# Kernel optimization log

Measured on AMD Instinct MI355X. Metric: run time of the kernel, lower is better.

Reference implementation:

```python
import jax, jax.numpy as jnp
import numpy as np

N_TF = 11
H = 1024
B = 2048


def setup_inputs() -> dict:
    key = jax.random.key(0)
    ks = jax.random.split(key, 10)
    s = 0.02  # weight init scale
    return {
        "h_stack": jax.random.normal(ks[0], (B, N_TF, H), dtype=jnp.float32),
        "base_confidence": jax.random.uniform(ks[1], (B,), dtype=jnp.float32),
        "kW1": jax.random.normal(ks[2], (H, H // 2), dtype=jnp.float32) * s,
        "kb1": jnp.zeros((H // 2,), jnp.float32),
        "kW2": jax.random.normal(ks[3], (H // 2, 1), dtype=jnp.float32) * s,
        "kb2": jnp.zeros((1,), jnp.float32),
        "lW1": jax.random.normal(ks[4], (H, H // 2), dtype=jnp.float32) * s,
        "lb1": jnp.zeros((H // 2,), jnp.float32),
        "lW2": jax.random.normal(ks[5], (H // 2, 1), dtype=jnp.float32) * s,
        "lb2": jnp.zeros((1,), jnp.float32),
        "dW1": jax.random.normal(ks[6], (2 * H, H), dtype=jnp.float32) * s,
        "db1": jnp.zeros((H,), jnp.float32),
        "dW2": jax.random.normal(ks[7], (H, 1), dtype=jnp.float32) * s,
        "db2": jnp.zeros((1,), jnp.float32),
        "kinetic_weight": jnp.asarray(1.0, jnp.float32),
        "local_weight": jnp.asarray(0.5, jnp.float32),
        "interaction_weight": jnp.asarray(0.3, jnp.float32),
        "temperature": jnp.asarray(1.0, jnp.float32),
    }


def reference(h_stack, base_confidence, kW1, kb1, kW2, kb2, lW1, lb1, lW2, lb2,
              dW1, db1, dW2, db2, kinetic_weight, local_weight,
              interaction_weight, temperature):
    n_tf = h_stack.shape[1]
    h = h_stack.shape[2]
    ii, jj = np.triu_indices(n_tf, k=1)  # 55 upper-triangular pairs
    dist_w = jnp.asarray(1.0 / (np.abs(ii - jj) + 1.0), dtype=h_stack.dtype)
    n_pairs = ii.shape[0]

    # kinetic: mean over TFs of small MLP, negated
    k_hid = jax.nn.relu(jnp.einsum('bth,hd->btd', h_stack, kW1) + kb1)
    k_per = (jnp.einsum('btd,do->bto', k_hid, kW2) + kb2)[..., 0]  # [B, T]
    kinetic_energy = -kinetic_weight * k_per.mean(axis=1)

    # local: relu of per-TF MLP, mean
    l_hid = jax.nn.relu(jnp.einsum('bth,hd->btd', h_stack, lW1) + lb1)
    l_per = (jnp.einsum('btd,do->bto', l_hid, lW2) + lb2)[..., 0]
    local_energy = local_weight * jax.nn.relu(l_per).mean(axis=1)

    # interaction: concat-MLP over all pairs, batched.
    # cat([h_i, h_j]) @ dW1 == h_i @ dW1[:H] + h_j @ dW1[H:]
    dW1a, dW1b = dW1[:h], dW1[h:]
    pre_i = jnp.einsum('bth,hd->btd', h_stack, dW1a)  # [B, T, H]
    pre_j = jnp.einsum('bth,hd->btd', h_stack, dW1b)  # [B, T, H]
    hid = jax.nn.relu(pre_i[:, ii] + pre_j[:, jj] + db1)  # [B, P, H]
    dis = jax.nn.relu((jnp.einsum('bpd,do->bpo', hid, dW2) + db2)[..., 0])  # [B, P]
    interaction_energy = interaction_weight * (dis * dist_w).sum(axis=1) / n_pairs

    total_energy = kinetic_energy + local_energy + interaction_energy
    energy_confidence = jax.nn.sigmoid(-total_energy / (jnp.abs(temperature) + 0.1))
    adjusted_confidence = base_confidence * energy_confidence
    return jnp.stack([total_energy, kinetic_energy, local_energy,
                      interaction_energy, energy_confidence,
                      adjusted_confidence], axis=0)  # [6, B]
```

## Files before the change

kernel.cpp:

```cpp
#include <hip/hip_runtime.h>
#include <hip/hip_bf16.h>
#include <math.h>

typedef __attribute__((ext_vector_type(8))) short bf16x8;
typedef __attribute__((ext_vector_type(4))) float f32x4;

#define NBATCH   2048
#define GB       4
#define ROWS     44
#define ROWSP    48
#define LDSA_BYTES (ROWSP * 1024 * 2)
#define STG_TILE   (ROWSP * 20)
#define STG_WAVE   (2 * STG_TILE)
#define LDS_TOTAL  (LDSA_BYTES + 8 * STG_WAVE * 4)

__device__ unsigned short g_wsB2[(size_t)3072 * 1024];

__device__ float g_ws2[(size_t)NBATCH * 128];

static constexpr int II_[55] = {
    0,0,0,0,0,0,0,0,0,0, 1,1,1,1,1,1,1,1,1, 2,2,2,2,2,2,2,2,
    3,3,3,3,3,3,3, 4,4,4,4,4,4, 5,5,5,5,5, 6,6,6,6, 7,7,7, 8,8, 9};
static constexpr int JJ_[55] = {
    1,2,3,4,5,6,7,8,9,10, 2,3,4,5,6,7,8,9,10, 3,4,5,6,7,8,9,10,
    4,5,6,7,8,9,10, 5,6,7,8,9,10, 6,7,8,9,10, 7,8,9,10, 8,9,10, 9,10, 10};

__device__ __forceinline__ unsigned short f32_to_bf16u(float f) {
    unsigned u = __float_as_uint(f);
    u += 0x7fffu + ((u >> 16) & 1u);
    return (unsigned short)(u >> 16);
}

__global__ void pack_weights(const float* __restrict__ kW1,
                             const float* __restrict__ lW1,
                             const float* __restrict__ dW1) {
    const int t = blockIdx.x * 256 + threadIdx.x;
    const int lane = t & 63;
    const int kk   = (t >> 6) & 31;
    const int g    = t >> 11;
    const int col  = g * 16 + (lane & 15);
    const int k0   = kk * 32 + (lane >> 4) * 8;
    const float* src; int ncol, c;
    if (col < 512)       { src = kW1;                          ncol = 512;  c = col; }
    else if (col < 1024) { src = lW1;                          ncol = 512;  c = col - 512; }
    else if (col < 2048) { src = dW1;                          ncol = 1024; c = col - 1024; }
    else                 { src = dW1 + (size_t)1024 * 1024;    ncol = 1024; c = col - 2048; }
    bf16x8 v;
    #pragma unroll
    for (int j = 0; j < 8; ++j)
        v[j] = (short)f32_to_bf16u(src[(size_t)(k0 + j) * ncol + c]);
    *(bf16x8*)(g_wsB2 + (size_t)t * 8) = v;
}

__launch_bounds__(512, 2)
__global__ void energy_mfma(
    const float* __restrict__ h_stack,
    const float* __restrict__ kb1, const float* __restrict__ kW2,
    const float* __restrict__ lb1, const float* __restrict__ lW2,
    const float* __restrict__ db1, const float* __restrict__ dW2)
{
    extern __shared__ char smem[];
    char* Ab = smem;
    float* stageBase = (float*)(smem + LDSA_BYTES);

    const int tid  = threadIdx.x;
    const int wv   = tid >> 6;
    const int ln   = tid & 63;
    const int lo16 = ln & 15;
    const int hi4  = ln >> 4;
    const unsigned xorv = (unsigned)((ln & 7) << 4);

    const int bx = blockIdx.x;
    const int x  = bx & 7;
    const int colHalf  = x & 1;
    const int rowBlock = (bx >> 3) * 4 + (x >> 1);

    {
        const size_t hbase = (size_t)rowBlock * (ROWS * 1024);
        #pragma unroll
        for (int i = 0; i < 11; ++i) {
            int idx = tid + i * 512;
            int row = idx >> 7;
            int kc  = idx & 127;
            const float* src = h_stack + hbase + (size_t)row * 1024 + kc * 8;
            float4 a = *(const float4*)src;
            float4 b = *(const float4*)(src + 4);
            bf16x8 v;
            v[0] = (short)f32_to_bf16u(a.x); v[1] = (short)f32_to_bf16u(a.y);
            v[2] = (short)f32_to_bf16u(a.z); v[3] = (short)f32_to_bf16u(a.w);
            v[4] = (short)f32_to_bf16u(b.x); v[5] = (short)f32_to_bf16u(b.y);
            v[6] = (short)f32_to_bf16u(b.z); v[7] = (short)f32_to_bf16u(b.w);
            unsigned kbyte = ((unsigned)(kc * 16)) ^ ((unsigned)((row & 7) << 4));
            *(bf16x8*)(Ab + row * 2048 + kbyte) = v;
        }
        {
            int row = ROWS + (tid >> 7);
            int kc  = tid & 127;
            unsigned kbyte = ((unsigned)(kc * 16)) ^ ((unsigned)((row & 7) << 4));
            bf16x8 z = {0,0,0,0,0,0,0,0};
            *(bf16x8*)(Ab + row * 2048 + kbyte) = z;
        }
    }
    __syncthreads();

    float kin_part = 0.f, loc_part = 0.f;
    float accP[55];
    #pragma unroll
    for (int p = 0; p < 55; ++p) accP[p] = 0.f;

    float* stg0 = stageBase + wv * STG_WAVE;
    float* stg1 = stg0 + STG_TILE;

    auto readA = [&](int m, int kk) -> bf16x8 {
        unsigned addr = (unsigned)((16 * m + lo16) * 2048)
                      + ((unsigned)(kk * 64 + hi4 * 16) ^ xorv);
        return *(const bf16x8*)(Ab + addr);
    };

    #pragma unroll 1
    for (int ui = 0; ui < 3; ++ui) {
        const int u = 24 * colHalf + ui * 8 + wv;
        int g0, g1, g2, g3;
        if (u < 16) { g0 = 4 * u; g1 = 4 * u + 1; g2 = 4 * u + 2; g3 = 4 * u + 3; }
        else        { int v = u - 16;
                      g0 = 64 + 2 * v; g1 = 128 + 2 * v;
                      g2 = 65 + 2 * v; g3 = 129 + 2 * v; }

        const unsigned short* bp0 = g_wsB2 + (size_t)g0 * 16384 + ln * 8;
        const unsigned short* bp1 = g_wsB2 + (size_t)g1 * 16384 + ln * 8;
        const unsigned short* bp2 = g_wsB2 + (size_t)g2 * 16384 + ln * 8;
        const unsigned short* bp3 = g_wsB2 + (size_t)g3 * 16384 + ln * 8;

        f32x4 acc[4][3];
        #pragma unroll
        for (int q = 0; q < 4; ++q)
            #pragma unroll
            for (int m = 0; m < 3; ++m) acc[q][m] = (f32x4){0.f, 0.f, 0.f, 0.f};

        auto ldB = [&](const unsigned short* p, int kk) -> bf16x8 {
            return *(const bf16x8*)(p + (size_t)kk * 512);
        };
        auto mfma12 = [&](bf16x8 a0, bf16x8 a1, bf16x8 a2,
                          bf16x8 b0, bf16x8 b1, bf16x8 b2, bf16x8 b3) {
            acc[0][0] = __builtin_amdgcn_mfma_f32_16x16x32_bf16(a0, b0, acc[0][0], 0, 0, 0);
            acc[0][1] = __builtin_amdgcn_mfma_f32_16x16x32_bf16(a1, b0, acc[0][1], 0, 0, 0);
            acc[0][2] = __builtin_amdgcn_mfma_f32_16x16x32_bf16(a2, b0, acc[0][2], 0, 0, 0);
            acc[1][0] = __builtin_amdgcn_mfma_f32_16x16x32_bf16(a0, b1, acc[1][0], 0, 0, 0);
            acc[1][1] = __builtin_amdgcn_mfma_f32_16x16x32_bf16(a1, b1, acc[1][1], 0, 0, 0);
            acc[1][2] = __builtin_amdgcn_mfma_f32_16x16x32_bf16(a2, b1, acc[1][2], 0, 0, 0);
            acc[2][0] = __builtin_amdgcn_mfma_f32_16x16x32_bf16(a0, b2, acc[2][0], 0, 0, 0);
            acc[2][1] = __builtin_amdgcn_mfma_f32_16x16x32_bf16(a1, b2, acc[2][1], 0, 0, 0);
            acc[2][2] = __builtin_amdgcn_mfma_f32_16x16x32_bf16(a2, b2, acc[2][2], 0, 0, 0);
            acc[3][0] = __builtin_amdgcn_mfma_f32_16x16x32_bf16(a0, b3, acc[3][0], 0, 0, 0);
            acc[3][1] = __builtin_amdgcn_mfma_f32_16x16x32_bf16(a1, b3, acc[3][1], 0, 0, 0);
            acc[3][2] = __builtin_amdgcn_mfma_f32_16x16x32_bf16(a2, b3, acc[3][2], 0, 0, 0);
        };

        bf16x8 A0 = readA(0, 0), A1 = readA(1, 0), A2 = readA(2, 0);
        bf16x8 B0 = ldB(bp0, 0), B1 = ldB(bp1, 0), B2 = ldB(bp2, 0), B3 = ldB(bp3, 0);
        bf16x8 C0 = ldB(bp0, 1), C1 = ldB(bp1, 1), C2 = ldB(bp2, 1), C3 = ldB(bp3, 1);

        #pragma unroll 2
        for (int kk = 0; kk < 31; ++kk) {
            bf16x8 a0 = A0, a1 = A1, a2 = A2;
            A0 = readA(0, kk + 1); A1 = readA(1, kk + 1); A2 = readA(2, kk + 1);
            bf16x8 b0 = B0, b1 = B1, b2 = B2, b3 = B3;
            B0 = C0; B1 = C1; B2 = C2; B3 = C3;
            if (kk < 30) {
                C0 = ldB(bp0, kk + 2); C1 = ldB(bp1, kk + 2);
                C2 = ldB(bp2, kk + 2); C3 = ldB(bp3, kk + 2);
            }
            mfma12(a0, a1, a2, b0, b1, b2, b3);
        }
        mfma12(A0, A1, A2, B0, B1, B2, B3);

        if (u < 16) {
            const float* b1arr = (u < 8) ? kb1 : lb1;
            const float* w2arr = (u < 8) ? kW2 : lW2;
            const int colrel0 = (u < 8) ? u * 64 : (u - 8) * 64;
            float part = 0.f;
            #pragma unroll
            for (int q = 0; q < 4; ++q) {
                const int colrel = colrel0 + q * 16 + lo16;
                const float b1v = b1arr[colrel];
                const float w2v = w2arr[colrel];
                float* sb = (q & 1) ? stg1 : stg0;
                #pragma unroll
                for (int m = 0; m < 3; ++m)
                    #pragma unroll
                    for (int r = 0; r < 4; ++r) {
                        const int row = 16 * m + 4 * hi4 + r;
                        sb[row * 20 + lo16] = fmaxf(acc[q][m][r] + b1v, 0.f) * w2v;
                    }
                asm volatile("s_waitcnt lgkmcnt(0)" ::: "memory");
                if (ln < ROWS) {
                    const f32x4* rp = (const f32x4*)(sb + ln * 20);
                    float s = 0.f;
                    #pragma unroll
                    for (int c4 = 0; c4 < 4; ++c4) {
                        f32x4 vv = rp[c4];
                        s += vv[0] + vv[1] + vv[2] + vv[3];
                    }
                    part += s;
                }
            }
            if (u < 8) kin_part += part; else loc_part += part;
        } else {
            const int v = u - 16;
            #pragma unroll
            for (int half = 0; half < 2; ++half) {
                const int dcol = (2 * v + half) * 16 + lo16;
                const float db1v = db1[dcol];
                const float dw2v = dW2[dcol];
                #pragma unroll
                for (int m = 0; m < 3; ++m)
                    #pragma unroll
                    for (int r = 0; r < 4; ++r) {
                        const int row = 16 * m + 4 * hi4 + r;
                        stg0[row * 20 + lo16] = acc[2 * half + 0][m][r];
                        stg1[row * 20 + lo16] = acc[2 * half + 1][m][r];
                    }
                asm volatile("s_waitcnt lgkmcnt(0)" ::: "memory");
                float pi[11], pj[11];
                #pragma unroll
                for (int t = 0; t < 11; ++t) {
                    const int row = 11 * hi4 + t;
                    pi[t] = stg0[row * 20 + lo16] + db1v;
                    pj[t] = stg1[row * 20 + lo16];
                }
                asm volatile("s_waitcnt lgkmcnt(0)" ::: "memory");
                #pragma unroll
                for (int p = 0; p < 55; ++p) {
                    const float s = pi[II_[p]] + pj[JJ_[p]];
                    accP[p] = fmaf(fmaxf(s, 0.f), dw2v, accP[p]);
                }
            }
        }
    }

    __syncthreads();
    float* kinbuf  = stageBase;
    float* locbuf  = stageBase + 512;
    float* pairbuf = stageBase + 1024;
    float* kinrow  = stageBase + 3040;
    float* locrow  = stageBase + 3104;

    kinbuf[wv * 64 + ln] = kin_part;
    locbuf[wv * 64 + ln] = loc_part;
    #pragma unroll
    for (int p = 0; p < 55; ++p) {
        float vsum = accP[p];
        vsum += __shfl_xor(vsum, 1);
        vsum += __shfl_xor(vsum, 2);
        vsum += __shfl_xor(vsum, 4);
        vsum += __shfl_xor(vsum, 8);
        if (lo16 == 0) pairbuf[wv * 224 + hi4 * 56 + p] = vsum;
    }
    __syncthreads();

    if (tid < 220) {
        const int b = tid / 55, p = tid % 55;
        float s = 0.f;
        #pragma unroll
        for (int w = 0; w < 8; ++w) s += pairbuf[w * 224 + b * 56 + p];
        const int gb = rowBlock * 4 + b;
        g_ws2[(size_t)gb * 128 + (colHalf ? 67 : 12) + p] = s;
    }
    if (colHalf == 0) {
        if (tid >= 256 && tid < 304) {
            const int r = tid - 256;
            float sk = 0.f, sl = 0.f;
            #pragma unroll
            for (int w = 0; w < 8; ++w) { sk += kinbuf[w * 64 + r]; sl += locbuf[w * 64 + r]; }
            kinrow[r] = sk; locrow[r] = sl;
        }
        __syncthreads();
        if (tid < 4) {
            const int b = tid;
            const int gb = rowBlock * 4 + b;
            float ks = 0.f;
            #pragma unroll
            for (int t = 0; t < 11; ++t) ks += kinrow[11 * b + t];
            g_ws2[(size_t)gb * 128 + 0] = ks;
            #pragma unroll
            for (int t = 0; t < 11; ++t)
                g_ws2[(size_t)gb * 128 + 1 + t] = locrow[11 * b + t];
        }
    }
}

__global__ void finalize(
    const float* __restrict__ base_conf,
    const float* __restrict__ kb2, const float* __restrict__ lb2,
    const float* __restrict__ db2,
    const float* __restrict__ kwp, const float* __restrict__ lwp,
    const float* __restrict__ iwp, const float* __restrict__ tmpp,
    float* __restrict__ out)
{
    const int gb = blockIdx.x * 256 + threadIdx.x;
    if (gb >= NBATCH) return;
    const float* w = g_ws2 + (size_t)gb * 128;
    const float kw = kwp[0], lw = lwp[0], iw = iwp[0], temp = tmpp[0];

    const float kinetic = -kw * (w[0] * (1.f / 11.f) + kb2[0]);

    float ls = 0.f;
    #pragma unroll
    for (int t = 0; t < 11; ++t) ls += fmaxf(w[1 + t] + lb2[0], 0.f);
    const float local_e = lw * (ls * (1.f / 11.f));

    float is = 0.f;
    #pragma unroll
    for (int p = 0; p < 55; ++p) {
        float s = w[12 + p] + w[67 + p] + db2[0];
        s = fmaxf(s, 0.f);
        is += s * (1.f / (float)(JJ_[p] - II_[p] + 1));
    }
    const float inter = iw * (is * (1.f / 55.f));

    const float total = kinetic + local_e + inter;
    const float ec = 1.f / (1.f + expf(total / (fabsf(temp) + 0.1f)));
    out[0 * NBATCH + gb] = total;
    out[1 * NBATCH + gb] = kinetic;
    out[2 * NBATCH + gb] = local_e;
    out[3 * NBATCH + gb] = inter;
    out[4 * NBATCH + gb] = ec;
    out[5 * NBATCH + gb] = base_conf[gb] * ec;
}

extern "C" void kernel_launch(void* const* d_in, const int* in_sizes, int n_in,
                              void* d_out, int out_size, void* d_ws, size_t ws_size,
                              hipStream_t stream) {
    const float* h_stack   = (const float*)d_in[0];
    const float* base_conf = (const float*)d_in[1];
    const float* kW1 = (const float*)d_in[2];
    const float* kb1 = (const float*)d_in[3];
    const float* kW2 = (const float*)d_in[4];
    const float* kb2 = (const float*)d_in[5];
    const float* lW1 = (const float*)d_in[6];
    const float* lb1 = (const float*)d_in[7];
    const float* lW2 = (const float*)d_in[8];
    const float* lb2 = (const float*)d_in[9];
    const float* dW1 = (const float*)d_in[10];
    const float* db1 = (const float*)d_in[11];
    const float* dW2 = (const float*)d_in[12];
    const float* db2 = (const float*)d_in[13];
    const float* kwp = (const float*)d_in[14];
    const float* lwp = (const float*)d_in[15];
    const float* iwp = (const float*)d_in[16];
    const float* tmpp= (const float*)d_in[17];
    float* out = (float*)d_out;

    hipLaunchKernelGGL(pack_weights, dim3(1536), dim3(256), 0, stream, kW1, lW1, dW1);

    hipFuncSetAttribute((const void*)energy_mfma,
                        hipFuncAttributeMaxDynamicSharedMemorySize, LDS_TOTAL);
    hipLaunchKernelGGL(energy_mfma, dim3(1024), dim3(512), LDS_TOTAL, stream,
                       h_stack, kb1, kW2, lb1, lW2, db1, dW2);

    hipLaunchKernelGGL(finalize, dim3(8), dim3(256), 0, stream,
                       base_conf, kb2, lb2, db2, kwp, lwp, iwp, tmpp, out);
}
```

Baseline: 289.2 us.

## Make energy kernel loop over four row blocks per workgroup

The grid shrinks from 1024 to 256 workgroups, and each workgroup now processes four consecutive row blocks in sequence. Each block gets its own h_stack staging, MFMA pass and reduction, with barriers between blocks. Launch bounds are relaxed to one workgroup per CU so the compiler has more registers, and h_stack is read with nontemporal loads. The aim is to cut workgroup launch and tail overhead and reduce register pressure, but staging the next block is still serialized with compute.

```diff
diff --git a/kernel.cpp b/kernel.cpp
--- a/kernel.cpp
+++ b/kernel.cpp
@@ -6,7 +6,6 @@
 typedef __attribute__((ext_vector_type(4))) float f32x4;
 
 #define NBATCH   2048
-#define GB       4
 #define ROWS     44
 #define ROWSP    48
 #define LDSA_BYTES (ROWSP * 1024 * 2)
@@ -29,6 +28,10 @@
     unsigned u = __float_as_uint(f);
     u += 0x7fffu + ((u >> 16) & 1u);
     return (unsigned short)(u >> 16);
+}
+
+__device__ __forceinline__ f32x4 ldnt(const float* p) {
+    return __builtin_nontemporal_load((const f32x4*)p);
 }
 
 __global__ void pack_weights(const float* __restrict__ kW1,
@@ -52,7 +55,7 @@
     *(bf16x8*)(g_wsB2 + (size_t)t * 8) = v;
 }
 
-__launch_bounds__(512, 2)
+__launch_bounds__(512, 1)
 __global__ void energy_mfma(
     const float* __restrict__ h_stack,
     const float* __restrict__ kb1, const float* __restrict__ kW2,
@@ -72,41 +75,39 @@
 
     const int bx = blockIdx.x;
     const int x  = bx & 7;
-    const int colHalf  = x & 1;
-    const int rowBlock = (bx >> 3) * 4 + (x >> 1);
-
-    {
-        const size_t hbase = (size_t)rowBlock * (ROWS * 1024);
+    const int colHalf = x & 1;
+    const int hidx    = (bx >> 3) * 4 + (x >> 1);
+    const int rbBase  = hidx * 4;
+
+    auto stageA = [&](int rb) {
+        const size_t hbase = (size_t)rb * (ROWS * 1024);
         #pragma unroll
         for (int i = 0; i < 11; ++i) {
             int idx = tid + i * 512;
             int row = idx >> 7;
             int kc  = idx & 127;
             const float* src = h_stack + hbase + (size_t)row * 1024 + kc * 8;
-            float4 a = *(const float4*)src;
-            float4 b = *(const float4*)(src + 4);
+            f32x4 a = ldnt(src);
+            f32x4 b = ldnt(src + 4);
             bf16x8 v;
-            v[0] = (short)f32_to_bf16u(a.x); v[1] = (short)f32_to_bf16u(a.y);
-            v[2] = (short)f32_to_bf16u(a.z); v[3] = (short)f32_to_bf16u(a.w);
-            v[4] = (short)f32_to_bf16u(b.x); v[5] = (short)f32_to_bf16u(b.y);
-            v[6] = (short)f32_to_bf16u(b.z); v[7] = (short)f32_to_bf16u(b.w);
+            v[0] = (short)f32_to_bf16u(a[0]); v[1] = (short)f32_to_bf16u(a[1]);
+            v[2] = (short)f32_to_bf16u(a[2]); v[3] = (short)f32_to_bf16u(a[3]);
+            v[4] = (short)f32_to_bf16u(b[0]); v[5] = (short)f32_to_bf16u(b[1]);
+            v[6] = (short)f32_to_bf16u(b[2]); v[7] = (short)f32_to_bf16u(b[3]);
             unsigned kbyte = ((unsigned)(kc * 16)) ^ ((unsigned)((row & 7) << 4));
             *(bf16x8*)(Ab + row * 2048 + kbyte) = v;
         }
-        {
-            int row = ROWS + (tid >> 7);
-            int kc  = tid & 127;
-            unsigned kbyte = ((unsigned)(kc * 16)) ^ ((unsigned)((row & 7) << 4));
-            bf16x8 z = {0,0,0,0,0,0,0,0};
-            *(bf16x8*)(Ab + row * 2048 + kbyte) = z;
-        }
+    };
+
+    {
+        int row = ROWS + (tid >> 7);
+        int kc  = tid & 127;
+        unsigned kbyte = ((unsigned)(kc * 16)) ^ ((unsigned)((row & 7) << 4));
+        bf16x8 z = {0,0,0,0,0,0,0,0};
+        *(bf16x8*)(Ab + row * 2048 + kbyte) = z;
     }
+    stageA(rbBase);
     __syncthreads();
-
-    float kin_part = 0.f, loc_part = 0.f;
-    float accP[55];
-    #pragma unroll
-    for (int p = 0; p < 55; ++p) accP[p] = 0.f;
 
     float* stg0 = stageBase + wv * STG_WAVE;
     float* stg1 = stg0 + STG_TILE;
@@ -118,173 +119,189 @@
     };
 
     #pragma unroll 1
-    for (int ui = 0; ui < 3; ++ui) {
-        const int u = 24 * colHalf + ui * 8 + wv;
-        int g0, g1, g2, g3;
-        if (u < 16) { g0 = 4 * u; g1 = 4 * u + 1; g2 = 4 * u + 2; g3 = 4 * u + 3; }
-        else        { int v = u - 16;
-                      g0 = 64 + 2 * v; g1 = 128 + 2 * v;
-                      g2 = 65 + 2 * v; g3 = 129 + 2 * v; }
-
-        const unsigned short* bp0 = g_wsB2 + (size_t)g0 * 16384 + ln * 8;
-        const unsigned short* bp1 = g_wsB2 + (size_t)g1 * 16384 + ln * 8;
-        const unsigned short* bp2 = g_wsB2 + (size_t)g2 * 16384 + ln * 8;
-        const unsigned short* bp3 = g_wsB2 + (size_t)g3 * 16384 + ln * 8;
-
-        f32x4 acc[4][3];
+    for (int item = 0; item < 4; ++item) {
+        const int rb = rbBase + item;
+
+        float kin_part = 0.f, loc_part = 0.f;
+        float accP[55];
         #pragma unroll
-        for (int q = 0; q < 4; ++q)
+        for (int p = 0; p < 55; ++p) accP[p] = 0.f;
+
+        #pragma unroll 1
+        for (int ui = 0; ui < 3; ++ui) {
+            const int u = 24 * colHalf + ui * 8 + wv;
+            int g0, g1, g2, g3;
+            if (u < 16) { g0 = 4 * u; g1 = 4 * u + 1; g2 = 4 * u + 2; g3 = 4 * u + 3; }
+            else        { int v = u - 16;
+                          g0 = 64 + 2 * v; g1 = 128 + 2 * v;
+                          g2 = 65 + 2 * v; g3 = 129 + 2 * v; }
+
+            const unsigned short* bp0 = g_wsB2 + (size_t)g0 * 16384 + ln * 8;
+            const unsigned short* bp1 = g_wsB2 + (size_t)g1 * 16384 + ln * 8;
+            const unsigned short* bp2 = g_wsB2 + (size_t)g2 * 16384 + ln * 8;
+            const unsigned short* bp3 = g_wsB2 + (size_t)g3 * 16384 + ln * 8;
+
+            f32x4 acc[4][3];
             #pragma unroll
-            for (int m = 0; m < 3; ++m) acc[q][m] = (f32x4){0.f, 0.f, 0.f, 0.f};
-
-        auto ldB = [&](const unsigned short* p, int kk) -> bf16x8 {
-            return *(const bf16x8*)(p + (size_t)kk * 512);
-        };
-        auto mfma12 = [&](bf16x8 a0, bf16x8 a1, bf16x8 a2,
-                          bf16x8 b0, bf16x8 b1, bf16x8 b2, bf16x8 b3) {
-            acc[0][0] = __builtin_amdgcn_mfma_f32_16x16x32_bf16(a0, b0, acc[0][0], 0, 0, 0);
-            acc[0][1] = __builtin_amdgcn_mfma_f32_16x16x32_bf16(a1, b0, acc[0][1], 0, 0, 0);
-            acc[0][2] = __builtin_amdgcn_mfma_f32_16x16x32_bf16(a2, b0, acc[0][2], 0, 0, 0);
-            acc[1][0] = __builtin_amdgcn_mfma_f32_16x16x32_bf16(a0, b1, acc[1][0], 0, 0, 0);
-            acc[1][1] = __builtin_amdgcn_mfma_f32_16x16x32_bf16(a1, b1, acc[1][1], 0, 0, 0);
-            acc[1][2] = __builtin_amdgcn_mfma_f32_16x16x32_bf16(a2, b1, acc[1][2], 0, 0, 0);
-            acc[2][0] = __builtin_amdgcn_mfma_f32_16x16x32_bf16(a0, b2, acc[2][0], 0, 0, 0);
-            acc[2][1] = __builtin_amdgcn_mfma_f32_16x16x32_bf16(a1, b2, acc[2][1], 0, 0, 0);
-            acc[2][2] = __builtin_amdgcn_mfma_f32_16x16x32_bf16(a2, b2, acc[2][2], 0, 0, 0);
-            acc[3][0] = __builtin_amdgcn_mfma_f32_16x16x32_bf16(a0, b3, acc[3][0], 0, 0, 0);
-            acc[3][1] = __builtin_amdgcn_mfma_f32_16x16x32_bf16(a1, b3, acc[3][1], 0, 0, 0);
-            acc[3][2] = __builtin_amdgcn_mfma_f32_16x16x32_bf16(a2, b3, acc[3][2], 0, 0, 0);
-        };
-
-        bf16x8 A0 = readA(0, 0), A1 = readA(1, 0), A2 = readA(2, 0);
-        bf16x8 B0 = ldB(bp0, 0), B1 = ldB(bp1, 0), B2 = ldB(bp2, 0), B3 = ldB(bp3, 0);
-        bf16x8 C0 = ldB(bp0, 1), C1 = ldB(bp1, 1), C2 = ldB(bp2, 1), C3 = ldB(bp3, 1);
-
-        #pragma unroll 2
-        for (int kk = 0; kk < 31; ++kk) {
-            bf16x8 a0 = A0, a1 = A1, a2 = A2;
-            A0 = readA(0, kk + 1); A1 = readA(1, kk + 1); A2 = readA(2, kk + 1);
-            bf16x8 b0 = B0, b1 = B1, b2 = B2, b3 = B3;
-            B0 = C0; B1 = C1; B2 = C2; B3 = C3;
-            if (kk < 30) {
-                C0 = ldB(bp0, kk + 2); C1 = ldB(bp1, kk + 2);
-                C2 = ldB(bp2, kk + 2); C3 = ldB(bp3, kk + 2);
+            for (int q = 0; q < 4; ++q)
+                #pragma unroll
+                for (int m = 0; m < 3; ++m) acc[q][m] = (f32x4){0.f, 0.f, 0.f, 0.f};
+
+            auto ldB = [&](const unsigned short* p, int kk) -> bf16x8 {
+                return *(const bf16x8*)(p + (size_t)kk * 512);
+            };
+            auto mfma12 = [&](bf16x8 a0, bf16x8 a1, bf16x8 a2,
+                              bf16x8 b0, bf16x8 b1, bf16x8 b2, bf16x8 b3) {
+                acc[0][0] = __builtin_amdgcn_mfma_f32_16x16x32_bf16(a0, b0, acc[0][0], 0, 0, 0);
+                acc[0][1] = __builtin_amdgcn_mfma_f32_16x16x32_bf16(a1, b0, acc[0][1], 0, 0, 0);
+                acc[0][2] = __builtin_amdgcn_mfma_f32_16x16x32_bf16(a2, b0, acc[0][2], 0, 0, 0);
+                acc[1][0] = __builtin_amdgcn_mfma_f32_16x16x32_bf16(a0, b1, acc[1][0], 0, 0, 0);
+                acc[1][1] = __builtin_amdgcn_mfma_f32_16x16x32_bf16(a1, b1, acc[1][1], 0, 0, 0);
+                acc[1][2] = __builtin_amdgcn_mfma_f32_16x16x32_bf16(a2, b1, acc[1][2], 0, 0, 0);
+                acc[2][0] = __builtin_amdgcn_mfma_f32_16x16x32_bf16(a0, b2, acc[2][0], 0, 0, 0);
+                acc[2][1] = __builtin_amdgcn_mfma_f32_16x16x32_bf16(a1, b2, acc[2][1], 0, 0, 0);
+                acc[2][2] = __builtin_amdgcn_mfma_f32_16x16x32_bf16(a2, b2, acc[2][2], 0, 0, 0);
+                acc[3][0] = __builtin_amdgcn_mfma_f32_16x16x32_bf16(a0, b3, acc[3][0], 0, 0, 0);
+                acc[3][1] = __builtin_amdgcn_mfma_f32_16x16x32_bf16(a1, b3, acc[3][1], 0, 0, 0);
+                acc[3][2] = __builtin_amdgcn_mfma_f32_16x16x32_bf16(a2, b3, acc[3][2], 0, 0, 0);
+            };
+
+            bf16x8 A0 = readA(0, 0), A1 = readA(1, 0), A2 = readA(2, 0);
+            bf16x8 B0 = ldB(bp0, 0), B1 = ldB(bp1, 0), B2 = ldB(bp2, 0), B3 = ldB(bp3, 0);
+            bf16x8 C0 = ldB(bp0, 1), C1 = ldB(bp1, 1), C2 = ldB(bp2, 1), C3 = ldB(bp3, 1);
+
+            #pragma unroll 2
+            for (int kk = 0; kk < 31; ++kk) {
+                bf16x8 a0 = A0, a1 = A1, a2 = A2;
+                A0 = readA(0, kk + 1); A1 = readA(1, kk + 1); A2 = readA(2, kk + 1);
+                bf16x8 b0 = B0, b1 = B1, b2 = B2, b3 = B3;
+                B0 = C0; B1 = C1; B2 = C2; B3 = C3;
+                if (kk < 30) {
+                    C0 = ldB(bp0, kk + 2); C1 = ldB(bp1, kk + 2);
+                    C2 = ldB(bp2, kk + 2); C3 = ldB(bp3, kk + 2);
+                }
+                mfma12(a0, a1, a2, b0, b1, b2, b3);
             }
-            mfma12(a0, a1, a2, b0, b1, b2, b3);
-        }
-        mfma12(A0, A1, A2, B0, B1, B2, B3);
-
-        if (u < 16) {
-            const float* b1arr = (u < 8) ? kb1 : lb1;
-            const float* w2arr = (u < 8) ? kW2 : lW2;
-            const int colrel0 = (u < 8) ? u * 64 : (u - 8) * 64;
-            float part = 0.f;
-            #pragma unroll
-            for (int q = 0; q < 4; ++q) {
-                const int colrel = colrel0 + q * 16 + lo16;
-                const float b1v = b1arr[colrel];
-                const float w2v = w2arr[colrel];
-                float* sb = (q & 1) ? stg1 : stg0;
-                #pragma unroll
-                for (int m = 0; m < 3; ++m)
+            mfma12(A0, A1, A2, B0, B1, B2, B3);
+
+            if (u < 16) {
+                const float* b1arr = (u < 8) ? kb1 : lb1;
+                const float* w2arr = (u < 8) ? kW2 : lW2;
+                const int colrel0 = (u < 8) ? u * 64 : (u - 8) * 64;
+                float part = 0.f;
+                #pragma unroll
+                for (int q = 0; q < 4; ++q) {
+                    const int colrel = colrel0 + q * 16 + lo16;
+                    const float b1v = b1arr[colrel];
+                    const float w2v = w2arr[colrel];
+                    float* sb = (q & 1) ? stg1 : stg0;
                     #pragma unroll
-                    for (int r = 0; r < 4; ++r) {
-                        const int row = 16 * m + 4 * hi4 + r;
-                        sb[row * 20 + lo16] = fmaxf(acc[q][m][r] + b1v, 0.f) * w2v;
+                    for (int m = 0; m < 3; ++m)
+                        #pragma unroll
+                        for (int r = 0; r < 4; ++r) {
+                            const int row = 16 * m + 4 * hi4 + r;
+                            sb[row * 20 + lo16] = fmaxf(acc[q][m][r] + b1v, 0.f) * w2v;
+                        }
+                    asm volatile("s_waitcnt lgkmcnt(0)" ::: "memory");
+                    if (ln < ROWS) {
+                        const f32x4* rp = (const f32x4*)(sb + ln * 20);
+                        float s = 0.f;
+                        #pragma unroll
+                        for (int c4 = 0; c4 < 4; ++c4) {
+                            f32x4 vv = rp[c4];
+                            s += vv[0] + vv[1] + vv[2] + vv[3];
+                        }
+                        part += s;
                     }
-                asm volatile("s_waitcnt lgkmcnt(0)" ::: "memory");
-                if (ln < ROWS) {
-                    const f32x4* rp = (const f32x4*)(sb + ln * 20);
-                    float s = 0.f;
+                }
+                if (u < 8) kin_part += part; else loc_part += part;
+            } else {
+                const int v = u - 16;
+                #pragma unroll
+                for (int half = 0; half < 2; ++half) {
+                    const int dcol = (2 * v + half) * 16 + lo16;
+                    const float db1v = db1[dcol];
+                    const float dw2v = dW2[dcol];
                     #pragma unroll
-                    for (int c4 = 0; c4 < 4; ++c4) {
-                        f32x4 vv = rp[c4];
-                        s += vv[0] + vv[1] + vv[2] + vv[3];
+                    for (int m = 0; m < 3; ++m)
+                        #pragma unroll
+                        for (int r = 0; r < 4; ++r) {
+                            const int row = 16 * m + 4 * hi4 + r;
+                            stg0[row * 20 + lo16] = acc[2 * half + 0][m][r];
+                            stg1[row * 20 + lo16] = acc[2 * half + 1][m][r];
+                        }
+                    asm volatile("s_waitcnt lgkmcnt(0)" ::: "memory");
+                    float pi[11], pj[11];
+                    #pragma unroll
+                    for (int t = 0; t < 11; ++t) {
+                        const int row = 11 * hi4 + t;
+                        pi[t] = stg0[row * 20 + lo16] + db1v;
+                        pj[t] = stg1[row * 20 + lo16];
                     }
-                    part += s;
+                    asm volatile("s_waitcnt lgkmcnt(0)" ::: "memory");
+                    #pragma unroll
+                    for (int p = 0; p < 55; ++p) {
+                        const float s = pi[II_[p]] + pj[JJ_[p]];
+                        accP[p] = fmaf(fmaxf(s, 0.f), dw2v, accP[p]);
+                    }
                 }
             }
-            if (u < 8) kin_part += part; else loc_part += part;
-        } else {
-            const int v = u - 16;
+        }
+
+        __syncthreads();
+        float* kinbuf  = stageBase;
+        float* locbuf  = stageBase + 512;
+        float* pairbuf = stageBase + 1024;
+        float* kinrow  = stageBase + 3040;
+        float* locrow  = stageBase + 3104;
+
+        kinbuf[wv * 64 + ln] = kin_part;
+        locbuf[wv * 64 + ln] = loc_part;
+        #pragma unroll
+        for (int p = 0; p < 55; ++p) {
+            float vsum = accP[p];
+            vsum += __shfl_xor(vsum, 1);
+            vsum += __shfl_xor(vsum, 2);
+            vsum += __shfl_xor(vsum, 4);
+            vsum += __shfl_xor(vsum, 8);
+            if (lo16 == 0) pairbuf[wv * 224 + hi4 * 56 + p] = vsum;
+        }
+        __syncthreads();
+
+        if (tid < 220) {
+            const int b = tid / 55, p = tid % 55;
+            float s = 0.f;
             #pragma unroll
-            for (int half = 0; half < 2; ++half) {
-                const int dcol = (2 * v + half) * 16 + lo16;
-                const float db1v = db1[dcol];
-                const float dw2v = dW2[dcol];
-                #pragma unroll
-                for (int m = 0; m < 3; ++m)
-                    #pragma unroll
-                    for (int r = 0; r < 4; ++r) {
-                        const int row = 16 * m + 4 * hi4 + r;
-                        stg0[row * 20 + lo16] = acc[2 * half + 0][m][r];
-                        stg1[row * 20 + lo16] = acc[2 * half + 1][m][r];
-                    }
-                asm volatile("s_waitcnt lgkmcnt(0)" ::: "memory");
-                float pi[11], pj[11];
-                #pragma unroll
-                for (int t = 0; t < 11; ++t) {
-                    const int row = 11 * hi4 + t;
-                    pi[t] = stg0[row * 20 + lo16] + db1v;
-                    pj[t] = stg1[row * 20 + lo16];
-                }
-                asm volatile("s_waitcnt lgkmcnt(0)" ::: "memory");
-                #pragma unroll
-                for (int p = 0; p < 55; ++p) {
-                    const float s = pi[II_[p]] + pj[JJ_[p]];
-                    accP[p] = fmaf(fmaxf(s, 0.f), dw2v, accP[p]);
-                }
+            for (int w = 0; w < 8; ++w) s += pairbuf[w * 224 + b * 56 + p];
+            const int gb = rb * 4 + b;
+            g_ws2[(size_t)gb * 128 + (colHalf ? 67 : 12) + p] = s;
+        }
+        if (colHalf == 0) {
+            if (tid >= 256 && tid < 304) {
+                const int r = tid - 256;
+                float sk = 0.f, sl = 0.f;
+                #pragma unroll
+                for (int w = 0; w < 8; ++w) { sk += kinbuf[w * 64 + r]; sl += locbuf[w * 64 + r]; }
+                kinrow[r] = sk; locrow[r] = sl;
             }
-        }
-    }
-
-    __syncthreads();
-    float* kinbuf  = stageBase;
-    float* locbuf  = stageBase + 512;
-    float* pairbuf = stageBase + 1024;
-    float* kinrow  = stageBase + 3040;
-    float* locrow  = stageBase + 3104;
-
-    kinbuf[wv * 64 + ln] = kin_part;
-    locbuf[wv * 64 + ln] = loc_part;
-    #pragma unroll
-    for (int p = 0; p < 55; ++p) {
-        float vsum = accP[p];
-        vsum += __shfl_xor(vsum, 1);
-        vsum += __shfl_xor(vsum, 2);
-        vsum += __shfl_xor(vsum, 4);
-        vsum += __shfl_xor(vsum, 8);
-        if (lo16 == 0) pairbuf[wv * 224 + hi4 * 56 + p] = vsum;
-    }
-    __syncthreads();
-
-    if (tid < 220) {
-        const int b = tid / 55, p = tid % 55;
-        float s = 0.f;
-        #pragma unroll
-        for (int w = 0; w < 8; ++w) s += pairbuf[w * 224 + b * 56 + p];
-        const int gb = rowBlock * 4 + b;
-        g_ws2[(size_t)gb * 128 + (colHalf ? 67 : 12) + p] = s;
-    }
-    if (colHalf == 0) {
-        if (tid >= 256 && tid < 304) {
-            const int r = tid - 256;
-            float sk = 0.f, sl = 0.f;
-            #pragma unroll
-            for (int w = 0; w < 8; ++w) { sk += kinbuf[w * 64 + r]; sl += locbuf[w * 64 + r]; }
-            kinrow[r] = sk; locrow[r] = sl;
+            __syncthreads();
+            if (tid < 4) {
+                const int b = tid;
+                const int gb = rb * 4 + b;
+                float ks = 0.f;
+                #pragma unroll
+                for (int t = 0; t < 11; ++t) ks += kinrow[11 * b + t];
+                g_ws2[(size_t)gb * 128 + 0] = ks;
+                #pragma unroll
+                for (int t = 0; t < 11; ++t)
+                    g_ws2[(size_t)gb * 128 + 1 + t] = locrow[11 * b + t];
+            }
         }
         __syncthreads();
-        if (tid < 4) {
-            const int b = tid;
-            const int gb = rowBlock * 4 + b;
-            float ks = 0.f;
-            #pragma unroll
-            for (int t = 0; t < 11; ++t) ks += kinrow[11 * b + t];
-            g_ws2[(size_t)gb * 128 + 0] = ks;
-            #pragma unroll
-            for (int t = 0; t < 11; ++t)
-                g_ws2[(size_t)gb * 128 + 1 + t] = locrow[11 * b + t];
+
+        if (item < 3) {
+            stageA(rb + 1);
+            __syncthreads();
         }
     }
 }
@@ -355,7 +372,7 @@
 
     hipFuncSetAttribute((const void*)energy_mfma,
                         hipFuncAttributeMaxDynamicSharedMemorySize, LDS_TOTAL);
-    hipLaunchKernelGGL(energy_mfma, dim3(1024), dim3(512), LDS_TOTAL, stream,
+    hipLaunchKernelGGL(energy_mfma, dim3(256), dim3(512), LDS_TOTAL, stream,
                        h_stack, kb1, kW2, lb1, lW2, db1, dW2);
 
     hipLaunchKernelGGL(finalize, dim3(8), dim3(256), 0, stream,
```

Result: slower. 325.1 us (+12.4%).
